# Optimization experiments

Measured on AMD Instinct MI355X. Metric: run time of the kernel, lower is better.

The kernel has to match this reference:

```python
import jax, jax.numpy as jnp
import numpy as np

H, W = 512, 512
N = H * W
NCLS = 4
D_BI, D_SP = 5, 2
THETA_ALPHA, THETA_BETA, THETA_GAMMA = 80.0, 0.0625, 3.0
BI_COMPAT, SP_COMPAT, COMPATIBILITY = 10.0, 3.0, -1.0
NUM_ITER = 10


def _build_lattice(feats):
    """Permutohedral lattice precompute (numpy, integer index construction).
    feats: [N, d]. Returns os [N,d+1] int32 (1-based), ws [N,d+1] float32,
    bn [d+1, M, 2] int32 (0 = missing neighbor), M."""
    feats = np.asarray(feats, np.float64)
    n, d = feats.shape
    inv_std = np.sqrt(2.0 / 3.0) * (d + 1)
    scale = inv_std / np.sqrt((np.arange(d) + 1.0) * (np.arange(d) + 2.0))
    cf = feats * scale
    # embedding matrix E: elevated = cf @ E.T lies on the hyperplane sum=0
    E = np.zeros((d + 1, d))
    E[0, :] = 1.0
    for j in range(1, d + 1):
        E[j, j:] = 1.0
        E[j, j - 1] = -j
    elevated = cf @ E.T  # [n, d+1]
    greedy = (np.rint(elevated / (d + 1)) * (d + 1)).astype(np.int64)
    diff = elevated - greedy
    idx = np.arange(d + 1)
    upper = idx[None, :] > idx[:, None]
    lower = idx[None, :] < idx[:, None]
    di = diff[:, :, None]
    dj = diff[:, None, :]
    rank = (((dj > di) & upper) | ((dj >= di) & lower)).sum(-1)
    rank = rank + greedy.sum(1, keepdims=True) // (d + 1)
    low = rank < 0
    rank = rank + np.where(low, d + 1, 0)
    greedy = greedy + np.where(low, d + 1, 0)
    high = rank > d
    rank = rank - np.where(high, d + 1, 0)
    greedy = greedy - np.where(high, d + 1, 0)
    # barycentric weights
    bary = np.zeros((n, d + 2))
    v = (elevated - greedy) / (d + 1)
    rows = np.repeat(np.arange(n), d + 1)
    np.add.at(bary, (rows, (d - rank).ravel()), v.ravel())
    np.add.at(bary, (rows, (d + 1 - rank).ravel()), -v.ravel())
    bary[:, 0] += 1.0 + bary[:, d + 1]
    ws = bary[:, : d + 1].astype(np.float32)
    # simplex vertex keys (first d coords; last is implied by zero-sum)
    keys = np.empty((n, d + 1, d), np.int64)
    for r in range(d + 1):
        keys[:, r, :] = (greedy + r - (d + 1) * (rank > d - r))[:, :d]
    flat = keys.reshape(-1, d)
    lo = flat.min(0) - (d + 1)
    hi = flat.max(0) + (d + 1)
    strides = np.cumprod(np.concatenate([[1], (hi - lo + 1)[:-1]]))
    coords = (flat - lo) @ strides
    uniq, first, inv = np.unique(coords, return_index=True, return_inverse=True)
    M = int(len(uniq))
    os_ = (inv.reshape(n, d + 1) + 1).astype(np.int32)
    ukeys = flat[first]
    bn = np.zeros((d + 1, M, 2), np.int32)
    for j in range(d + 1):
        n1 = ukeys - 1
        n2 = ukeys + 1
        if j < d:
            n1[:, j] = ukeys[:, j] + d
            n2[:, j] = ukeys[:, j] - d
        for t, nk in enumerate((n1, n2)):
            c = (nk - lo) @ strides
            pos = np.clip(np.searchsorted(uniq, c), 0, M - 1)
            bn[j, :, t] = np.where(uniq[pos] == c, pos + 1, 0)
    return os_, ws, bn, M


def setup_inputs() -> dict:
    key = jax.random.key(0)
    k1, k2 = jax.random.split(key)
    image = jax.random.uniform(k1, (H, W, 7), dtype=jnp.float32)
    unary = jax.random.normal(k2, (H, W, NCLS), dtype=jnp.float32)
    img = np.asarray(image)
    yy, xx = np.mgrid[0:H, 0:W].astype(np.float64)
    bifeat = np.concatenate(
        [(xx / THETA_ALPHA)[..., None], (yy / THETA_ALPHA)[..., None],
         img[..., :3] / THETA_BETA], axis=-1).reshape(N, D_BI)
    spfeat = np.stack([xx / THETA_GAMMA, yy / THETA_GAMMA], -1).reshape(N, D_SP)
    os_b, ws_b, bn_b, M_b = _build_lattice(bifeat)
    os_s, ws_s, bn_s, M_s = _build_lattice(spfeat)
    return {
        "unary": unary,
        "ws_bilateral": jnp.asarray(ws_b), "os_bilateral": jnp.asarray(os_b),
        "blur_neighbors_bilateral": jnp.asarray(bn_b), "M_bilateral": M_b,
        "ws_spatial": jnp.asarray(ws_s), "os_spatial": jnp.asarray(os_s),
        "blur_neighbors_spatial": jnp.asarray(bn_s), "M_spatial": M_s,
    }


def _perm_filter(values, os_, ws, bn, M, alpha):
    # values: [N, C]; splat -> blur -> slice
    d1 = os_.shape[1]
    C = values.shape[1]
    table = jnp.zeros((M + 1, C), values.dtype)  # row 0 = dummy (missing)
    table = table.at[os_.reshape(-1)].add(
        (values[:, None, :] * ws[:, :, None]).reshape(-1, C))
    for j in range(d1):  # [0.5, 1, 0.5] blur along each lattice axis
        table = table.at[1:].add(0.5 * (table[bn[j, :, 0]] + table[bn[j, :, 1]]))
    return alpha * jnp.einsum("nrc,nr->nc", table[os_], ws)


def _mean_field(unary, ws_b, os_b, bn_b, M_b, ws_s, os_s, bn_s, M_s):
    C = unary.shape[-1]
    u = unary.reshape(N, C)
    alpha_b = 1.0 / (1.0 + 2.0 ** (-D_BI))
    alpha_s = 1.0 / (1.0 + 2.0 ** (-D_SP))
    ones = jnp.ones((N, 1), u.dtype)
    inv_nb = 1.0 / (_perm_filter(ones, os_b, ws_b, bn_b, M_b, alpha_b) + 1e-20)
    inv_ns = 1.0 / (_perm_filter(ones, os_s, ws_s, bn_s, M_s, alpha_s) + 1e-20)
    Q = jax.nn.softmax(-u, axis=-1)
    for _ in range(NUM_ITER):
        msg = (BI_COMPAT * _perm_filter(Q, os_b, ws_b, bn_b, M_b, alpha_b) * inv_nb
               + SP_COMPAT * _perm_filter(Q, os_s, ws_s, bn_s, M_s, alpha_s) * inv_ns)
        Q = jax.nn.softmax(-u - COMPATIBILITY * msg, axis=-1)
    return Q.reshape(H, W, C)


def reference(unary, ws_bilateral, os_bilateral, blur_neighbors_bilateral, M_bilateral,
              ws_spatial, os_spatial, blur_neighbors_spatial, M_spatial):
    # Returns the refined marginals Q [H, W, NCLS]; the module's MAP output is
    # jnp.argmax(Q, -1) (kept soft here so fwd/bwd share one output).
    return _mean_field(unary, ws_bilateral, os_bilateral, blur_neighbors_bilateral,
                       M_bilateral, ws_spatial, os_spatial, blur_neighbors_spatial,
                       M_spatial)
```

## Files before the change

### kernel.cpp

```cpp
#include <hip/hip_runtime.h>

#define NPIX (512 * 512)
#define BLK 256

#define TOTB (NPIX * 6)
#define TOTS (NPIX * 3)
#define TOTE (NPIX * 9)

typedef _Float16 h4 __attribute__((ext_vector_type(4)));

constexpr float ALPHA_B = 32.0f / 33.0f;
constexpr float ALPHA_S = 0.8f;
constexpr float BI_COMPAT = 10.0f;
constexpr float SP_COMPAT = 3.0f;

__device__ __forceinline__ unsigned pack_ent(int n, float w) {
    float wc = fminf(fmaxf(w, 0.f), 1.f);
    unsigned iw = (unsigned)(wc * 16383.f + 0.5f);
    return (iw << 18) | (unsigned)n;
}
__device__ __forceinline__ int ent_pix(unsigned e) { return (int)(e & 0x3FFFFu); }
__device__ __forceinline__ float ent_w(unsigned e) {
    return (float)(e >> 18) * (1.0f / 16383.0f);
}

__device__ __forceinline__ float4 f4zero() { return make_float4(0.f, 0.f, 0.f, 0.f); }
__device__ __forceinline__ h4 h4zero() {
    h4 z; z.x = (_Float16)0.f; z.y = (_Float16)0.f; z.z = (_Float16)0.f; z.w = (_Float16)0.f;
    return z;
}

__global__ void k_softmax_init(const float4* __restrict__ u, float4* __restrict__ Q) {
    int n = blockIdx.x * BLK + threadIdx.x;
    if (n >= NPIX) return;
    float4 uu = u[n];
    float l0 = -uu.x, l1 = -uu.y, l2 = -uu.z, l3 = -uu.w;
    float m = fmaxf(fmaxf(l0, l1), fmaxf(l2, l3));
    float e0 = expf(l0 - m), e1 = expf(l1 - m), e2 = expf(l2 - m), e3 = expf(l3 - m);
    float inv = 1.0f / (e0 + e1 + e2 + e3);
    Q[n] = make_float4(e0 * inv, e1 * inv, e2 * inv, e3 * inv);
}

__global__ void k_link_softmax(const int* __restrict__ osb, const int* __restrict__ oss,
                               int* __restrict__ head, int* __restrict__ next,
                               const float4* __restrict__ u, float4* __restrict__ Q,
                               int Vb) {
    int n = blockIdx.x * BLK + threadIdx.x;
    if (n >= NPIX) return;
    float4 uu = u[n];
    float l0 = -uu.x, l1 = -uu.y, l2 = -uu.z, l3 = -uu.w;
    float m = fmaxf(fmaxf(l0, l1), fmaxf(l2, l3));
    float e0 = expf(l0 - m), e1 = expf(l1 - m), e2 = expf(l2 - m), e3 = expf(l3 - m);
    float inv = 1.0f / (e0 + e1 + e2 + e3);
    Q[n] = make_float4(e0 * inv, e1 * inv, e2 * inv, e3 * inv);
#pragma unroll
    for (int r = 0; r < 6; r++) {
        int o = osb[n * 6 + r];
        int e = n * 6 + r;
        next[e] = atomicExch(&head[o], e);
    }
#pragma unroll
    for (int r = 0; r < 3; r++) {
        int o = Vb + oss[n * 3 + r];
        int e = TOTB + n * 3 + r;
        next[e] = atomicExch(&head[o], e);
    }
}

__global__ void k_compact(const int* __restrict__ head, const int* __restrict__ next,
                          const float* __restrict__ wsb, const float* __restrict__ wss,
                          unsigned* __restrict__ ent, int* __restrict__ start,
                          int* __restrict__ endv,
                          float* __restrict__ nB, float* __restrict__ nS,
                          int* __restrict__ cursor, int V, int Vb) {
    __shared__ int lds[BLK];
    __shared__ int sbase;
    int o = blockIdx.x * BLK + threadIdx.x;
    bool valid = o < V;
    int h = valid ? head[o] : -1;
    int len = 0;
    for (int e = h; e >= 0; e = next[e]) len++;
    lds[threadIdx.x] = len;
    __syncthreads();
    for (int off = 1; off < BLK; off <<= 1) {
        int t = ((int)threadIdx.x >= off) ? lds[threadIdx.x - off] : 0;
        __syncthreads();
        lds[threadIdx.x] += t;
        __syncthreads();
    }
    int incl = lds[threadIdx.x];
    if (threadIdx.x == BLK - 1) sbase = atomicAdd(cursor, incl);
    __syncthreads();
    if (!valid) return;
    int pos = sbase + incl - len;
    start[o] = pos;
    endv[o] = pos + len;
    float acc = 0.f;
    if (o < Vb) {
        for (int e = h; e >= 0; e = next[e]) {
            unsigned n = (unsigned)e / 6u;
            unsigned pe = pack_ent((int)n, wsb[e]);
            acc += ent_w(pe);
            ent[pos++] = pe;
        }
        nB[o] = acc;
    } else {
        for (int e = h; e >= 0; e = next[e]) {
            int ee = e - TOTB;
            unsigned pe = pack_ent(ee / 3, wss[ee]);
            acc += ent_w(pe);
            ent[pos++] = pe;
        }
        nS[o - Vb] = acc;
    }
}

__global__ void k_gather4h_both(const unsigned* __restrict__ ent, const int* __restrict__ start,
                                const int* __restrict__ endv, int V, int Vb,
                                h4* __restrict__ tB, h4* __restrict__ tS,
                                const float4* __restrict__ Q) {
    int i = blockIdx.x * BLK + threadIdx.x;
    if (i >= V) return;
    int s = start[i];
    int e = endv[i];
    float ax = 0.f, ay = 0.f, az = 0.f, aw = 0.f;
    for (int k = s; k < e; k++) {
        unsigned en = ent[k];
        float w = ent_w(en);
        float4 q = Q[ent_pix(en)];
        ax += w * q.x; ay += w * q.y; az += w * q.z; aw += w * q.w;
    }
    h4 h;
    h.x = (_Float16)ax; h.y = (_Float16)ay; h.z = (_Float16)az; h.w = (_Float16)aw;
    if (i < Vb) tB[i] = h;
    else tS[i - Vb] = h;
}

__global__ void k_blur1(const float* __restrict__ in, float* __restrict__ out,
                        const int* __restrict__ bn, int M) {
    int i = blockIdx.x * BLK + threadIdx.x;
    if (i > M) return;
    if (i == 0) { out[0] = 0.f; return; }
    int n1 = bn[(size_t)(i - 1) * 2 + 0];
    int n2 = bn[(size_t)(i - 1) * 2 + 1];
    out[i] = in[i] + 0.5f * (in[n1] + in[n2]);
}

__global__ void k_blur1_both(const float* __restrict__ inB, float* __restrict__ outB,
                             const int* __restrict__ bnB, int Mb,
                             const float* __restrict__ inS, float* __restrict__ outS,
                             const int* __restrict__ bnS, int Ms) {
    int i = blockIdx.x * BLK + threadIdx.x;
    const float* in; float* out; const int* bn; int M, idx;
    if (i <= Mb) { in = inB; out = outB; bn = bnB; M = Mb; idx = i; }
    else {
        idx = i - (Mb + 1);
        if (idx > Ms) return;
        in = inS; out = outS; bn = bnS; M = Ms;
    }
    if (idx == 0) { out[0] = 0.f; return; }
    int n1 = bn[(size_t)(idx - 1) * 2 + 0];
    int n2 = bn[(size_t)(idx - 1) * 2 + 1];
    out[idx] = in[idx] + 0.5f * (in[n1] + in[n2]);
}

__global__ void k_blur4h(const h4* __restrict__ in, h4* __restrict__ out,
                         const int* __restrict__ bn, int M) {
    int i = blockIdx.x * BLK + threadIdx.x;
    if (i > M) return;
    if (i == 0) { out[0] = h4zero(); return; }
    int n1 = bn[(size_t)(i - 1) * 2 + 0];
    int n2 = bn[(size_t)(i - 1) * 2 + 1];
    h4 a = in[i], b = in[n1], c = in[n2];
    h4 o;
    o.x = (_Float16)((float)a.x + 0.5f * ((float)b.x + (float)c.x));
    o.y = (_Float16)((float)a.y + 0.5f * ((float)b.y + (float)c.y));
    o.z = (_Float16)((float)a.z + 0.5f * ((float)b.z + (float)c.z));
    o.w = (_Float16)((float)a.w + 0.5f * ((float)b.w + (float)c.w));
    out[i] = o;
}

__global__ void k_blur4h_both(const h4* __restrict__ inB, h4* __restrict__ outB,
                              const int* __restrict__ bnB, int Mb,
                              const h4* __restrict__ inS, h4* __restrict__ outS,
                              const int* __restrict__ bnS, int Ms) {
    int i = blockIdx.x * BLK + threadIdx.x;
    const h4* in; h4* out; const int* bn; int M, idx;
    if (i <= Mb) { in = inB; out = outB; bn = bnB; M = Mb; idx = i; }
    else {
        idx = i - (Mb + 1);
        if (idx > Ms) return;
        in = inS; out = outS; bn = bnS; M = Ms;
    }
    if (idx == 0) { out[0] = h4zero(); return; }
    int n1 = bn[(size_t)(idx - 1) * 2 + 0];
    int n2 = bn[(size_t)(idx - 1) * 2 + 1];
    h4 a = in[idx], b = in[n1], c = in[n2];
    h4 o;
    o.x = (_Float16)((float)a.x + 0.5f * ((float)b.x + (float)c.x));
    o.y = (_Float16)((float)a.y + 0.5f * ((float)b.y + (float)c.y));
    o.z = (_Float16)((float)a.z + 0.5f * ((float)b.z + (float)c.z));
    o.w = (_Float16)((float)a.w + 0.5f * ((float)b.w + (float)c.w));
    out[idx] = o;
}

__global__ void k_norm_prescale(const float* __restrict__ nTb, const float* __restrict__ wsb,
                                const int* __restrict__ osb,
                                const float* __restrict__ nTs, const float* __restrict__ wss,
                                const int* __restrict__ oss,
                                float* __restrict__ wsbp, float* __restrict__ wssp) {
    int n = blockIdx.x * BLK + threadIdx.x;
    if (n >= NPIX) return;
    float sb = 0.f;
#pragma unroll
    for (int r = 0; r < 6; r++) sb += wsb[n * 6 + r] * nTb[osb[n * 6 + r]];
    float cb = BI_COMPAT * ALPHA_B / (ALPHA_B * sb + 1e-20f);
#pragma unroll
    for (int r = 0; r < 6; r++) wsbp[n * 6 + r] = wsb[n * 6 + r] * cb;
    float ss = 0.f;
#pragma unroll
    for (int r = 0; r < 3; r++) ss += wss[n * 3 + r] * nTs[oss[n * 3 + r]];
    float cs = SP_COMPAT * ALPHA_S / (ALPHA_S * ss + 1e-20f);
#pragma unroll
    for (int r = 0; r < 3; r++) wssp[n * 3 + r] = wss[n * 3 + r] * cs;
}

__global__ void k_slice_combine_h(const float4* __restrict__ u,
                                  const h4* __restrict__ tb, const float* __restrict__ wsbp,
                                  const int* __restrict__ osb,
                                  const h4* __restrict__ ts, const float* __restrict__ wssp,
                                  const int* __restrict__ oss,
                                  float4* __restrict__ Qout) {
    int n = blockIdx.x * BLK + threadIdx.x;
    if (n >= NPIX) return;
    float4 uu = u[n];
    float l0 = -uu.x, l1 = -uu.y, l2 = -uu.z, l3 = -uu.w;
#pragma unroll
    for (int r = 0; r < 6; r++) {
        float w = wsbp[n * 6 + r];
        h4 t = tb[osb[n * 6 + r]];
        l0 += w * (float)t.x; l1 += w * (float)t.y; l2 += w * (float)t.z; l3 += w * (float)t.w;
    }
#pragma unroll
    for (int r = 0; r < 3; r++) {
        float w = wssp[n * 3 + r];
        h4 t = ts[oss[n * 3 + r]];
        l0 += w * (float)t.x; l1 += w * (float)t.y; l2 += w * (float)t.z; l3 += w * (float)t.w;
    }
    float m = fmaxf(fmaxf(l0, l1), fmaxf(l2, l3));
    float e0 = expf(l0 - m), e1 = expf(l1 - m), e2 = expf(l2 - m), e3 = expf(l3 - m);
    float inv = 1.0f / (e0 + e1 + e2 + e3);
    Qout[n] = make_float4(e0 * inv, e1 * inv, e2 * inv, e3 * inv);
}

template <int D1>
__global__ void k_splat1(const float* __restrict__ ws, const int* __restrict__ os,
                         float* __restrict__ table) {
    int n = blockIdx.x * BLK + threadIdx.x;
    if (n >= NPIX) return;
#pragma unroll
    for (int r = 0; r < D1; r++) atomicAdd(&table[os[n * D1 + r]], ws[n * D1 + r]);
}

template <int D1>
__global__ void k_splat4(const float4* __restrict__ Q, const float* __restrict__ ws,
                         const int* __restrict__ os, float* __restrict__ table) {
    int n = blockIdx.x * BLK + threadIdx.x;
    if (n >= NPIX) return;
    float4 q = Q[n];
#pragma unroll
    for (int r = 0; r < D1; r++) {
        float w = ws[n * D1 + r];
        int o = os[n * D1 + r];
        float* t = table + 4 * (size_t)o;
        atomicAdd(t + 0, q.x * w);
        atomicAdd(t + 1, q.y * w);
        atomicAdd(t + 2, q.z * w);
        atomicAdd(t + 3, q.w * w);
    }
}

__global__ void k_blur4(const float4* __restrict__ in, float4* __restrict__ out,
                        const int* __restrict__ bn, int M) {
    int i = blockIdx.x * BLK + threadIdx.x;
    if (i > M) return;
    if (i == 0) { out[0] = f4zero(); return; }
    int n1 = bn[(size_t)(i - 1) * 2 + 0];
    int n2 = bn[(size_t)(i - 1) * 2 + 1];
    float4 a = in[i], b = in[n1], c = in[n2];
    out[i] = make_float4(a.x + 0.5f * (b.x + c.x), a.y + 0.5f * (b.y + c.y),
                         a.z + 0.5f * (b.z + c.z), a.w + 0.5f * (b.w + c.w));
}

template <int D1>
__global__ void k_norm_slice(const float* __restrict__ table, const float* __restrict__ ws,
                             const int* __restrict__ os, float alpha,
                             float* __restrict__ inv_out) {
    int n = blockIdx.x * BLK + threadIdx.x;
    if (n >= NPIX) return;
    float s = 0.f;
#pragma unroll
    for (int r = 0; r < D1; r++) s += ws[n * D1 + r] * table[os[n * D1 + r]];
    inv_out[n] = 1.0f / (alpha * s + 1e-20f);
}

__global__ void k_slice_combine(const float4* __restrict__ u,
                                const float4* __restrict__ tb, const float* __restrict__ wsb,
                                const int* __restrict__ osb,
                                const float4* __restrict__ ts, const float* __restrict__ wss,
                                const int* __restrict__ oss,
                                const float* __restrict__ inv_nb,
                                const float* __restrict__ inv_ns,
                                float4* __restrict__ Qout) {
    int n = blockIdx.x * BLK + threadIdx.x;
    if (n >= NPIX) return;
    float4 ab = f4zero();
#pragma unroll
    for (int r = 0; r < 6; r++) {
        float w = wsb[n * 6 + r];
        float4 t = tb[osb[n * 6 + r]];
        ab.x += w * t.x; ab.y += w * t.y; ab.z += w * t.z; ab.w += w * t.w;
    }
    float4 as = f4zero();
#pragma unroll
    for (int r = 0; r < 3; r++) {
        float w = wss[n * 3 + r];
        float4 t = ts[oss[n * 3 + r]];
        as.x += w * t.x; as.y += w * t.y; as.z += w * t.z; as.w += w * t.w;
    }
    float cb = BI_COMPAT * ALPHA_B * inv_nb[n];
    float cs = SP_COMPAT * ALPHA_S * inv_ns[n];
    float4 uu = u[n];
    float l0 = -uu.x + cb * ab.x + cs * as.x;
    float l1 = -uu.y + cb * ab.y + cs * as.y;
    float l2 = -uu.z + cb * ab.z + cs * as.z;
    float l3 = -uu.w + cb * ab.w + cs * as.w;
    float m = fmaxf(fmaxf(l0, l1), fmaxf(l2, l3));
    float e0 = expf(l0 - m), e1 = expf(l1 - m), e2 = expf(l2 - m), e3 = expf(l3 - m);
    float inv = 1.0f / (e0 + e1 + e2 + e3);
    Qout[n] = make_float4(e0 * inv, e1 * inv, e2 * inv, e3 * inv);
}

extern "C" void kernel_launch(void* const* d_in, const int* in_sizes, int n_in,
                              void* d_out, int out_size, void* d_ws, size_t ws_size,
                              hipStream_t stream) {
    const float* unary = (const float*)d_in[0];
    const float* wsb   = (const float*)d_in[1];
    const int*   osb   = (const int*)d_in[2];
    const int*   bnb   = (const int*)d_in[3];
    const float* wss   = (const float*)d_in[5];
    const int*   oss   = (const int*)d_in[6];
    const int*   bns   = (const int*)d_in[7];
    const int Mb = in_sizes[3] / 12;
    const int Ms = in_sizes[7] / 6;
    const int Vb = Mb + 1, Vs = Ms + 1;
    const int V = Vb + Vs;

    float* Q = (float*)d_out;

    char* p = (char*)d_ws;
    auto alloc = [&](size_t nbytes) -> void* {
        void* r = (void*)p;
        p += (nbytes + 15) & ~(size_t)15;
        return r;
    };
    h4*   tAb  = (h4*)alloc((size_t)Vb * 8);
    h4*   tBb  = (h4*)alloc((size_t)Vb * 8);
    h4*   tAs  = (h4*)alloc((size_t)Vs * 8);
    h4*   tBs  = (h4*)alloc((size_t)Vs * 8);
    float* nAb = (float*)alloc((size_t)Vb * 4);
    float* nBb = (float*)alloc((size_t)Vb * 4);
    float* nAs = (float*)alloc((size_t)Vs * 4);
    float* nBs = (float*)alloc((size_t)Vs * 4);
    float* wsbp = (float*)alloc((size_t)NPIX * 6 * 4);
    float* wssp = (float*)alloc((size_t)NPIX * 3 * 4);
    int*   next = (int*)wsbp;
    int*  start = (int*)alloc((size_t)V * 4);
    int*  endv  = (int*)alloc((size_t)V * 4);
    int*  head  = (int*)alloc((size_t)V * 4);
    unsigned* ent = (unsigned*)alloc((size_t)TOTE * 4);
    int*  cursor = (int*)alloc(16);
    size_t need = (size_t)(p - (char*)d_ws);
    bool use_gather = need <= ws_size;

    dim3 blk(BLK);
    dim3 gN((NPIX + BLK - 1) / BLK);
    dim3 gVb((Vb + BLK - 1) / BLK);
    dim3 gV((V + BLK - 1) / BLK);

    if (use_gather) {
        hipMemsetAsync(head, 0xFF, (size_t)V * 4, stream);
        hipMemsetAsync(cursor, 0, 16, stream);
        k_link_softmax<<<gN, blk, 0, stream>>>(osb, oss, head, next,
                                               (const float4*)unary, (float4*)Q, Vb);
        k_compact<<<gV, blk, 0, stream>>>(head, next, wsb, wss, ent, start, endv,
                                          nAb, nAs, cursor, V, Vb);

        {
            float* a = nAb; float* b = nBb;
            float* as_ = nAs; float* bs_ = nBs;
            for (int j = 0; j < 3; j++) {
                k_blur1_both<<<gV, blk, 0, stream>>>(a, b, bnb + (size_t)j * Mb * 2, Mb,
                                                     as_, bs_, bns + (size_t)j * Ms * 2, Ms);
                float* t = a; a = b; b = t;
                t = as_; as_ = bs_; bs_ = t;
            }
            for (int j = 3; j < 6; j++) {
                k_blur1<<<gVb, blk, 0, stream>>>(a, b, bnb + (size_t)j * Mb * 2, Mb);
                float* t = a; a = b; b = t;
            }
            k_norm_prescale<<<gN, blk, 0, stream>>>(a, wsb, osb, as_, wss, oss, wsbp, wssp);
        }

        for (int it = 0; it < 10; it++) {
            k_gather4h_both<<<gV, blk, 0, stream>>>(ent, start, endv, V, Vb, tAb, tAs,
                                                    (const float4*)Q);
            h4* a = tAb; h4* b = tBb;
            h4* as_ = tAs; h4* bs_ = tBs;
            for (int j = 0; j < 3; j++) {
                k_blur4h_both<<<gV, blk, 0, stream>>>(a, b, bnb + (size_t)j * Mb * 2, Mb,
                                                      as_, bs_, bns + (size_t)j * Ms * 2, Ms);
                h4* t = a; a = b; b = t;
                t = as_; as_ = bs_; bs_ = t;
            }
            for (int j = 3; j < 6; j++) {
                k_blur4h<<<gVb, blk, 0, stream>>>(a, b, bnb + (size_t)j * Mb * 2, Mb);
                h4* t = a; a = b; b = t;
            }
            k_slice_combine_h<<<gN, blk, 0, stream>>>((const float4*)unary,
                                                      a, wsbp, osb, as_, wssp, oss,
                                                      (float4*)Q);
        }
    } else {
        char* q = (char*)d_ws;
        auto alloc2 = [&](size_t nbytes) -> void* {
            void* r = (void*)q;
            q += (nbytes + 15) & ~(size_t)15;
            return r;
        };
        float* fAb = (float*)alloc2((size_t)Vb * 4 * sizeof(float));
        float* fBb = (float*)alloc2((size_t)Vb * 4 * sizeof(float));
        float* fAs = (float*)alloc2((size_t)Vs * 4 * sizeof(float));
        float* fBs = (float*)alloc2((size_t)Vs * 4 * sizeof(float));
        float* inv_nb = (float*)alloc2(NPIX * sizeof(float));
        float* inv_ns = (float*)alloc2(NPIX * sizeof(float));
        dim3 gMb((Mb + 1 + BLK - 1) / BLK);
        dim3 gMs((Ms + 1 + BLK - 1) / BLK);

        hipMemsetAsync(fAb, 0, (size_t)Vb * sizeof(float), stream);
        k_splat1<6><<<gN, blk, 0, stream>>>(wsb, osb, fAb);
        {
            float* a = fAb; float* b = fBb;
            for (int j = 0; j < 6; j++) {
                k_blur1<<<gMb, blk, 0, stream>>>(a, b, bnb + (size_t)j * Mb * 2, Mb);
                float* t = a; a = b; b = t;
            }
            k_norm_slice<6><<<gN, blk, 0, stream>>>(a, wsb, osb, ALPHA_B, inv_nb);
        }
        hipMemsetAsync(fAs, 0, (size_t)Vs * sizeof(float), stream);
        k_splat1<3><<<gN, blk, 0, stream>>>(wss, oss, fAs);
        {
            float* a = fAs; float* b = fBs;
            for (int j = 0; j < 3; j++) {
                k_blur1<<<gMs, blk, 0, stream>>>(a, b, bns + (size_t)j * Ms * 2, Ms);
                float* t = a; a = b; b = t;
            }
            k_norm_slice<3><<<gN, blk, 0, stream>>>(a, wss, oss, ALPHA_S, inv_ns);
        }
        k_softmax_init<<<gN, blk, 0, stream>>>((const float4*)unary, (float4*)Q);
        for (int it = 0; it < 10; it++) {
            hipMemsetAsync(fAb, 0, (size_t)Vb * 4 * sizeof(float), stream);
            k_splat4<6><<<gN, blk, 0, stream>>>((const float4*)Q, wsb, osb, fAb);
            float* a = fAb; float* b = fBb;
            for (int j = 0; j < 6; j++) {
                k_blur4<<<gMb, blk, 0, stream>>>((const float4*)a, (float4*)b,
                                                 bnb + (size_t)j * Mb * 2, Mb);
                float* t = a; a = b; b = t;
            }
            float* finb = a;
            hipMemsetAsync(fAs, 0, (size_t)Vs * 4 * sizeof(float), stream);
            k_splat4<3><<<gN, blk, 0, stream>>>((const float4*)Q, wss, oss, fAs);
            float* as_ = fAs; float* bs_ = fBs;
            for (int j = 0; j < 3; j++) {
                k_blur4<<<gMs, blk, 0, stream>>>((const float4*)as_, (float4*)bs_,
                                                 bns + (size_t)j * Ms * 2, Ms);
                float* t = as_; as_ = bs_; bs_ = t;
            }
            float* fins = as_;
            k_slice_combine<<<gN, blk, 0, stream>>>((const float4*)unary,
                                                    (const float4*)finb, wsb, osb,
                                                    (const float4*)fins, wss, oss,
                                                    inv_nb, inv_ns, (float4*)Q);
        }
    }
}
```

Before: 952.4 us.

## Build vertex lists with wave-coalesced atomics and packed 64-bit nodes

Replaces the per-entry linked-list build with a wavefront-level scheme. Consecutive lanes that hit the same lattice vertex are chained locally, so only the run head does an atomicExch. Each node stores the next index and the packed pixel/weight payload in one 64-bit word, so compaction walks one array and does not re-read os/ws. The workspace is reordered so the 8-byte node array fits in reused buffers, with the old path kept as a fallback. The blur launch grid is also recomputed, which adds a little indexing complexity.

After: 940.5 us. No clear change (-1.2%).

```diff
diff --git a/kernel.cpp b/kernel.cpp
--- a/kernel.cpp
+++ b/kernel.cpp
@@ -8,6 +8,7 @@
 #define TOTE (NPIX * 9)
 
 typedef _Float16 h4 __attribute__((ext_vector_type(4)));
+typedef unsigned long long u64;
 
 constexpr float ALPHA_B = 32.0f / 33.0f;
 constexpr float ALPHA_S = 0.8f;
@@ -22,6 +23,9 @@
 __device__ __forceinline__ int ent_pix(unsigned e) { return (int)(e & 0x3FFFFu); }
 __device__ __forceinline__ float ent_w(unsigned e) {
     return (float)(e >> 18) * (1.0f / 16383.0f);
+}
+__device__ __forceinline__ u64 mknode(int nxt, unsigned pay) {
+    return ((u64)(unsigned)nxt << 32) | (u64)pay;
 }
 
 __device__ __forceinline__ float4 f4zero() { return make_float4(0.f, 0.f, 0.f, 0.f); }
@@ -39,6 +43,88 @@
     float e0 = expf(l0 - m), e1 = expf(l1 - m), e2 = expf(l2 - m), e3 = expf(l3 - m);
     float inv = 1.0f / (e0 + e1 + e2 + e3);
     Q[n] = make_float4(e0 * inv, e1 * inv, e2 * inv, e3 * inv);
+}
+
+template <int D1>
+__device__ __forceinline__ void link_slot(const int* __restrict__ os, const float* __restrict__ ws,
+                                          int* __restrict__ head, u64* __restrict__ next2,
+                                          int n, int r, int obase, int ebase, int lane) {
+    int o = obase + os[n * D1 + r];
+    int e = ebase + n * D1 + r;
+    unsigned pay = pack_ent(n, ws[n * D1 + r]);
+    int o_prev = __shfl_up(o, 1);
+    bool is_head = (lane == 0) || (o != o_prev);
+    u64 hm = __ballot(is_head);
+    u64 above = (hm >> lane) >> 1;
+    int runlen = above ? __ffsll((long long)above) : (64 - lane);
+    int e_prevlane = __shfl_up(e, 1);
+    u64 node;
+    if (is_head) {
+        int e_last = e + (runlen - 1) * D1;
+        int old = atomicExch(&head[o], e_last);
+        node = mknode(old, pay);
+    } else {
+        node = mknode(e_prevlane, pay);
+    }
+    next2[e] = node;
+}
+
+__global__ void k_link2_softmax(const int* __restrict__ osb, const float* __restrict__ wsb,
+                                const int* __restrict__ oss, const float* __restrict__ wss,
+                                int* __restrict__ head, u64* __restrict__ next2,
+                                const float4* __restrict__ u, float4* __restrict__ Q,
+                                int Vb) {
+    int n = blockIdx.x * BLK + threadIdx.x;
+    float4 uu = u[n];
+    float l0 = -uu.x, l1 = -uu.y, l2 = -uu.z, l3 = -uu.w;
+    float m = fmaxf(fmaxf(l0, l1), fmaxf(l2, l3));
+    float e0 = expf(l0 - m), e1 = expf(l1 - m), e2 = expf(l2 - m), e3 = expf(l3 - m);
+    float inv = 1.0f / (e0 + e1 + e2 + e3);
+    Q[n] = make_float4(e0 * inv, e1 * inv, e2 * inv, e3 * inv);
+    int lane = threadIdx.x & 63;
+#pragma unroll
+    for (int r = 0; r < 6; r++) link_slot<6>(osb, wsb, head, next2, n, r, 0, 0, lane);
+#pragma unroll
+    for (int r = 0; r < 3; r++) link_slot<3>(oss, wss, head, next2, n, r, Vb, TOTB, lane);
+}
+
+__global__ void k_compact2(const int* __restrict__ head, const u64* __restrict__ next2,
+                           unsigned* __restrict__ ent, int* __restrict__ start,
+                           int* __restrict__ endv,
+                           float* __restrict__ nB, float* __restrict__ nS,
+                           int* __restrict__ cursor, int V, int Vb) {
+    __shared__ int lds[BLK];
+    __shared__ int sbase;
+    int o = blockIdx.x * BLK + threadIdx.x;
+    bool valid = o < V;
+    int h = valid ? head[o] : -1;
+    int len = 0;
+    for (int e = h; e >= 0;) { e = (int)(next2[e] >> 32); len++; }
+    lds[threadIdx.x] = len;
+    __syncthreads();
+    for (int off = 1; off < BLK; off <<= 1) {
+        int t = ((int)threadIdx.x >= off) ? lds[threadIdx.x - off] : 0;
+        __syncthreads();
+        lds[threadIdx.x] += t;
+        __syncthreads();
+    }
+    int incl = lds[threadIdx.x];
+    if (threadIdx.x == BLK - 1) sbase = atomicAdd(cursor, incl);
+    __syncthreads();
+    if (!valid) return;
+    int pos = sbase + incl - len;
+    start[o] = pos;
+    endv[o] = pos + len;
+    float acc = 0.f;
+    for (int e = h; e >= 0;) {
+        u64 nd = next2[e];
+        unsigned pe = (unsigned)nd;
+        acc += ent_w(pe);
+        ent[pos++] = pe;
+        e = (int)(nd >> 32);
+    }
+    if (o < Vb) nB[o] = acc;
+    else nS[o - Vb] = acc;
 }
 
 __global__ void k_link_softmax(const int* __restrict__ osb, const int* __restrict__ oss,
@@ -364,17 +450,18 @@
         p += (nbytes + 15) & ~(size_t)15;
         return r;
     };
+    char* region0 = p;
+    float* wsbp = (float*)alloc((size_t)NPIX * 6 * 4);
+    float* wssp = (float*)alloc((size_t)NPIX * 3 * 4);
     h4*   tAb  = (h4*)alloc((size_t)Vb * 8);
     h4*   tBb  = (h4*)alloc((size_t)Vb * 8);
     h4*   tAs  = (h4*)alloc((size_t)Vs * 8);
     h4*   tBs  = (h4*)alloc((size_t)Vs * 8);
+    float* nBb = (float*)alloc((size_t)Vb * 4);
+    float* nBs = (float*)alloc((size_t)Vs * 4);
+    size_t region_bytes = (size_t)(p - region0);
     float* nAb = (float*)alloc((size_t)Vb * 4);
-    float* nBb = (float*)alloc((size_t)Vb * 4);
     float* nAs = (float*)alloc((size_t)Vs * 4);
-    float* nBs = (float*)alloc((size_t)Vs * 4);
-    float* wsbp = (float*)alloc((size_t)NPIX * 6 * 4);
-    float* wssp = (float*)alloc((size_t)NPIX * 3 * 4);
-    int*   next = (int*)wsbp;
     int*  start = (int*)alloc((size_t)V * 4);
     int*  endv  = (int*)alloc((size_t)V * 4);
     int*  head  = (int*)alloc((size_t)V * 4);
@@ -382,26 +469,37 @@
     int*  cursor = (int*)alloc(16);
     size_t need = (size_t)(p - (char*)d_ws);
     bool use_gather = need <= ws_size;
+    bool use8 = region_bytes >= (size_t)TOTE * 8;
+    u64*  next2 = (u64*)region0;
+    int*  next4 = (int*)region0;
 
     dim3 blk(BLK);
     dim3 gN((NPIX + BLK - 1) / BLK);
     dim3 gVb((Vb + BLK - 1) / BLK);
     dim3 gV((V + BLK - 1) / BLK);
+    dim3 gVBS((Vb + Vs + 1 + BLK - 1) / BLK);
 
     if (use_gather) {
         hipMemsetAsync(head, 0xFF, (size_t)V * 4, stream);
         hipMemsetAsync(cursor, 0, 16, stream);
-        k_link_softmax<<<gN, blk, 0, stream>>>(osb, oss, head, next,
-                                               (const float4*)unary, (float4*)Q, Vb);
-        k_compact<<<gV, blk, 0, stream>>>(head, next, wsb, wss, ent, start, endv,
-                                          nAb, nAs, cursor, V, Vb);
+        if (use8) {
+            k_link2_softmax<<<gN, blk, 0, stream>>>(osb, wsb, oss, wss, head, next2,
+                                                    (const float4*)unary, (float4*)Q, Vb);
+            k_compact2<<<gV, blk, 0, stream>>>(head, next2, ent, start, endv,
+                                               nAb, nAs, cursor, V, Vb);
+        } else {
+            k_link_softmax<<<gN, blk, 0, stream>>>(osb, oss, head, next4,
+                                                   (const float4*)unary, (float4*)Q, Vb);
+            k_compact<<<gV, blk, 0, stream>>>(head, next4, wsb, wss, ent, start, endv,
+                                              nAb, nAs, cursor, V, Vb);
+        }
 
         {
             float* a = nAb; float* b = nBb;
             float* as_ = nAs; float* bs_ = nBs;
             for (int j = 0; j < 3; j++) {
-                k_blur1_both<<<gV, blk, 0, stream>>>(a, b, bnb + (size_t)j * Mb * 2, Mb,
-                                                     as_, bs_, bns + (size_t)j * Ms * 2, Ms);
+                k_blur1_both<<<gVBS, blk, 0, stream>>>(a, b, bnb + (size_t)j * Mb * 2, Mb,
+                                                       as_, bs_, bns + (size_t)j * Ms * 2, Ms);
                 float* t = a; a = b; b = t;
                 t = as_; as_ = bs_; bs_ = t;
             }
@@ -418,8 +516,8 @@
             h4* a = tAb; h4* b = tBb;
             h4* as_ = tAs; h4* bs_ = tBs;
             for (int j = 0; j < 3; j++) {
-                k_blur4h_both<<<gV, blk, 0, stream>>>(a, b, bnb + (size_t)j * Mb * 2, Mb,
-                                                      as_, bs_, bns + (size_t)j * Ms * 2, Ms);
+                k_blur4h_both<<<gVBS, blk, 0, stream>>>(a, b, bnb + (size_t)j * Mb * 2, Mb,
+                                                        as_, bs_, bns + (size_t)j * Ms * 2, Ms);
                 h4* t = a; a = b; b = t;
                 t = as_; as_ = bs_; bs_ = t;
             }
```
